# Performance work log

Hardware: AMD Instinct MI355X
Metric: run time of the kernel (lower is better)

## Reference

```python
import jax, jax.numpy as jnp
import numpy as np

POOLED_H = 7
POOLED_W = 7
SPATIAL_SCALE = 0.0625
IMG = 896  # image size -> 56x56 feature map at stride 16


def setup_inputs() -> dict:
    key = jax.random.key(0)
    kf, kb, kx1, kx2, ky1, ky2 = jax.random.split(key, 6)
    B, C, H, W = 4, 256, 56, 56
    N = 256
    features = jax.random.normal(kf, (B, C, H, W), dtype=jnp.float32)
    b = jax.random.randint(kb, (N,), 0, B)
    x1 = jax.random.randint(kx1, (N,), 0, IMG)
    y1 = jax.random.randint(ky1, (N,), 0, IMG)
    x2 = jnp.clip(x1 + jax.random.randint(kx2, (N,), 0, IMG), None, IMG - 1)
    y2 = jnp.clip(y1 + jax.random.randint(ky2, (N,), 0, IMG), None, IMG - 1)
    rois = jnp.stack([b, x1, y1, x2, y2], axis=1).astype(jnp.float32)
    return {"features": features, "rois": rois}


def reference(features, rois):
    # Faithful RoIPool (pool_type='MAX'):
    #   rois[:,1:] *= spatial_scale; rois = rois.long()  (truncation; coords >= 0 so == floor)
    #   crop features[b, :, y1:y2+1, x1:x2+1] and adaptive_max_pool2d to (7,7).
    B, C, H, W = features.shape
    N = rois.shape[0]
    r = rois.at[:, 1:].multiply(SPATIAL_SCALE).astype(jnp.int32)
    b, x1, y1, x2, y2 = r[:, 0], r[:, 1], r[:, 2], r[:, 3], r[:, 4]
    roi_h = y2 - y1 + 1  # crop uses y2+1 inclusive end
    roi_w = x2 - x1 + 1
    # adaptive pool bins for length L, out size o: start=floor(i*L/o), end=ceil((i+1)*L/o)
    # max bin width is bounded by ceil(H/o)+1, a static quantity -> jit friendly.
    MBH = -(-H // POOLED_H) + 1
    MBW = -(-W // POOLED_W) + 1
    ph = jnp.arange(POOLED_H)
    pw = jnp.arange(POOLED_W)

    hs = y1[:, None] + (ph[None, :] * roi_h[:, None]) // POOLED_H              # [N,7]
    he = y1[:, None] + ((ph[None, :] + 1) * roi_h[:, None] + POOLED_H - 1) // POOLED_H
    kh = jnp.arange(MBH)
    h_idx = jnp.clip(hs[:, :, None] + kh, 0, H - 1)                            # [N,7,MBH]
    h_valid = kh[None, None, :] < (he - hs)[:, :, None]                        # [N,7,MBH]

    ws = x1[:, None] + (pw[None, :] * roi_w[:, None]) // POOLED_W              # [N,7]
    we = x1[:, None] + ((pw[None, :] + 1) * roi_w[:, None] + POOLED_W - 1) // POOLED_W
    kw = jnp.arange(MBW)
    w_idx = jnp.clip(ws[:, :, None] + kw, 0, W - 1)                            # [N,7,MBW]
    w_valid = kw[None, None, :] < (we - ws)[:, :, None]                        # [N,7,MBW]

    fb = features[b]  # [N,C,H,W] per-ROI feature maps
    # max over the rectangle is separable: max over rows, then over cols.
    gh = jax.vmap(lambda f, hi: f[:, hi, :])(fb, h_idx)                        # [N,C,7,MBH,W]
    gh = jnp.where(h_valid[:, None, :, :, None], gh, -jnp.inf).max(axis=3)     # [N,C,7,W]
    gw = jax.vmap(lambda f, wi: f[:, :, wi])(gh, w_idx)                        # [N,C,7,7,MBW]
    out = jnp.where(w_valid[:, None, None, :, :], gw, -jnp.inf).max(axis=-1)   # [N,C,7,7]
    return out
```

## Files before the change

### kernel.cpp

```cpp
#include <hip/hip_runtime.h>
#include <math.h>

#define POOLED 7
#define SCALE 0.0625f
#define C_ 256
#define H_ 56
#define W_ 56
#define S_ (H_ * W_)
#define NCELL 49

typedef _Float16 f16x4 __attribute__((ext_vector_type(4)));

__device__ __forceinline__ f16x4 max4h(f16x4 a, f16x4 b) {
    f16x4 r;
    r[0] = a[0] > b[0] ? a[0] : b[0];
    r[1] = a[1] > b[1] ? a[1] : b[1];
    r[2] = a[2] > b[2] ? a[2] : b[2];
    r[3] = a[3] > b[3] ? a[3] : b[3];
    return r;
}

__global__ __launch_bounds__(1024) void nhwc_kernel(
    const float* __restrict__ src, _Float16* __restrict__ dst)
{
    __shared__ float tile[64][65];
    int b = blockIdx.z;
    int sbase = blockIdx.x * 64;
    int cbase = blockIdx.y * 64;
    int tid = threadIdx.x;

    const float* s0 = src + (size_t)b * C_ * S_;
    _Float16* d0 = dst + (size_t)b * S_ * C_;

    {
        int si = tid & 15;
        int c  = tid >> 4;
        float4 v = *(const float4*)(s0 + (size_t)(cbase + c) * S_ + sbase + 4 * si);
        tile[4 * si + 0][c] = v.x;
        tile[4 * si + 1][c] = v.y;
        tile[4 * si + 2][c] = v.z;
        tile[4 * si + 3][c] = v.w;
    }
    __syncthreads();
    {
        int cj = tid & 15;
        int s  = tid >> 4;
        f16x4 pk;
        pk[0] = (_Float16)tile[s][4 * cj + 0];
        pk[1] = (_Float16)tile[s][4 * cj + 1];
        pk[2] = (_Float16)tile[s][4 * cj + 2];
        pk[3] = (_Float16)tile[s][4 * cj + 3];
        *(f16x4*)(d0 + (size_t)(sbase + s) * C_ + cbase + 4 * cj) = pk;
    }
}

__global__ __launch_bounds__(256) void pool_kernel(
    const _Float16* __restrict__ t, const float* __restrict__ rois,
    float* __restrict__ ws2)
{
    int bid  = blockIdx.x;
    int swz  = (bid & 7) * 392 + (bid >> 3);
    int task = (threadIdx.x >> 6) * 3136 + swz;
    int lane = threadIdx.x & 63;

    int n    = task / NCELL;
    int cell = task % NCELL;
    int ph = cell / POOLED;
    int pw = cell % POOLED;

    const float* r = rois + n * 5;
    int b  = (int)r[0];
    int x1 = (int)(r[1] * SCALE);
    int y1 = (int)(r[2] * SCALE);
    int x2 = (int)(r[3] * SCALE);
    int y2 = (int)(r[4] * SCALE);
    int rh = y2 - y1 + 1;
    int rw = x2 - x1 + 1;

    int hs = y1 + (ph * rh) / POOLED;
    int he = y1 + ((ph + 1) * rh + POOLED - 1) / POOLED;
    int ws = x1 + (pw * rw) / POOLED;
    int we = x1 + ((pw + 1) * rw + POOLED - 1) / POOLED;
    int nh = he - hs;
    int nw = we - ws;

    const f16x4* p0 = (const f16x4*)(t + (size_t)b * S_ * C_) + lane
                      + (size_t)(hs * W_ + ws) * 64;

    const _Float16 NEGV = (_Float16)(-65504.0f);
    f16x4 a0 = {NEGV, NEGV, NEGV, NEGV};
    f16x4 a1 = a0, a2 = a0, a3 = a0, a4 = a0, a5 = a0, a6 = a0, a7 = a0;

    for (int h = 0; h < nh; h += 2) {
        int h1 = (h + 1 < nh) ? h + 1 : h;
        const f16x4* hp0 = p0 + (size_t)h  * (W_ * 64);
        const f16x4* hp1 = p0 + (size_t)h1 * (W_ * 64);
        for (int w = 0; w < nw; w += 4) {
            int w1 = (w + 1 < nw) ? w + 1 : w;
            int w2 = (w + 2 < nw) ? w + 2 : w;
            int w3 = (w + 3 < nw) ? w + 3 : w;
            a0 = max4h(a0, hp0[(size_t)w  * 64]);
            a1 = max4h(a1, hp0[(size_t)w1 * 64]);
            a2 = max4h(a2, hp0[(size_t)w2 * 64]);
            a3 = max4h(a3, hp0[(size_t)w3 * 64]);
            a4 = max4h(a4, hp1[(size_t)w  * 64]);
            a5 = max4h(a5, hp1[(size_t)w1 * 64]);
            a6 = max4h(a6, hp1[(size_t)w2 * 64]);
            a7 = max4h(a7, hp1[(size_t)w3 * 64]);
        }
    }
    f16x4 m = max4h(max4h(max4h(a0, a1), max4h(a2, a3)),
                    max4h(max4h(a4, a5), max4h(a6, a7)));

    float4 acc = make_float4((float)m[0], (float)m[1], (float)m[2], (float)m[3]);
    *((float4*)(ws2 + (size_t)task * C_) + lane) = acc;
}

__global__ __launch_bounds__(256) void outt_kernel(
    const float* __restrict__ ws2, float* __restrict__ out)
{
    __shared__ float tile[64][51];
    int n = blockIdx.x;
    int cbase = blockIdx.y * 64;
    int tid = threadIdx.x;

    const float* src = ws2 + (size_t)n * NCELL * C_;
    int cl = tid & 63;
    int cell0 = tid >> 6;
    #pragma unroll
    for (int k = 0; k < 13; ++k) {
        int cell = cell0 + 4 * k;
        if (cell < NCELL) tile[cl][cell] = src[(size_t)cell * C_ + cbase + cl];
    }
    __syncthreads();
    float* dst = out + (size_t)n * C_ * NCELL + (size_t)cbase * NCELL;
    #pragma unroll
    for (int k = 0; k < 13; ++k) {
        int f = tid + 256 * k;
        if (f < 64 * NCELL) {
            int c = f / NCELL, cell = f % NCELL;
            dst[f] = tile[c][cell];
        }
    }
}

__global__ __launch_bounds__(256) void roipool_direct_kernel(
    const float* __restrict__ feat, const float* __restrict__ rois,
    float* __restrict__ out, int total)
{
    int idx = blockIdx.x * blockDim.x + threadIdx.x;
    if (idx >= total) return;
    int pw = idx % POOLED;
    int ph = (idx / POOLED) % POOLED;
    int c  = (idx / (POOLED * POOLED)) % C_;
    int n  = idx / (POOLED * POOLED * C_);
    const float* r = rois + n * 5;
    int b  = (int)r[0];
    int x1 = (int)(r[1] * SCALE);
    int y1 = (int)(r[2] * SCALE);
    int x2 = (int)(r[3] * SCALE);
    int y2 = (int)(r[4] * SCALE);
    int rh = y2 - y1 + 1;
    int rw = x2 - x1 + 1;
    int hs = y1 + (ph * rh) / POOLED;
    int he = y1 + ((ph + 1) * rh + POOLED - 1) / POOLED;
    int ws = x1 + (pw * rw) / POOLED;
    int we = x1 + ((pw + 1) * rw + POOLED - 1) / POOLED;
    const float* plane = feat + ((size_t)b * C_ + c) * (size_t)S_;
    float m = -INFINITY;
    for (int h = hs; h < he; ++h) {
        const float* row = plane + h * W_;
        for (int w = ws; w < we; ++w) m = fmaxf(m, row[w]);
    }
    out[idx] = m;
}

extern "C" void kernel_launch(void* const* d_in, const int* in_sizes, int n_in,
                              void* d_out, int out_size, void* d_ws, size_t ws_size,
                              hipStream_t stream) {
    const float* feat = (const float*)d_in[0];
    const float* rois = (const float*)d_in[1];
    float* out = (float*)d_out;

    int N = in_sizes[1] / 5;
    size_t featBytes = (size_t)4 * S_ * C_ * sizeof(_Float16);
    size_t need = featBytes + (size_t)N * NCELL * C_ * sizeof(float);

    if (ws_size >= need && N == 256) {
        _Float16* t = (_Float16*)d_ws;
        float* ws2  = (float*)((char*)d_ws + featBytes);

        dim3 tgrid(S_ / 64, C_ / 64, 4);
        nhwc_kernel<<<tgrid, 1024, 0, stream>>>(feat, t);

        pool_kernel<<<3136, 256, 0, stream>>>(t, rois, ws2);

        dim3 ogrid(N, C_ / 64);
        outt_kernel<<<ogrid, 256, 0, stream>>>(ws2, out);
    } else {
        int total = N * C_ * POOLED * POOLED;
        roipool_direct_kernel<<<(total + 255) / 256, 256, 0, stream>>>(feat, rois, out, total);
    }
}
```

Measured before the change: 34.82 us.

## Fuse pooling and output transpose into one kernel via shared-memory staging

Each block now handles one ROI and a group of four pooled cells, one wave per cell. Results are staged in shared memory and written straight to the NCHW-ordered output. This removes the intermediate workspace buffer, its global write and read, and one kernel launch. In exchange the output stores are strided by 49 floats, so they are poorly coalesced. The last cell group has three idle waves, and the grid grows to 3328 blocks.

```diff
diff --git a/kernel.cpp b/kernel.cpp
--- a/kernel.cpp
+++ b/kernel.cpp
@@ -54,19 +54,18 @@
     }
 }
 
-__global__ __launch_bounds__(256) void pool_kernel(
+__global__ __launch_bounds__(256) void pool_fused_kernel(
     const _Float16* __restrict__ t, const float* __restrict__ rois,
-    float* __restrict__ ws2)
+    float* __restrict__ out)
 {
-    int bid  = blockIdx.x;
-    int swz  = (bid & 7) * 392 + (bid >> 3);
-    int task = (threadIdx.x >> 6) * 3136 + swz;
+    __shared__ float stage[4][257];
+    int b0   = blockIdx.x;
+    int swz  = (b0 & 7) * 416 + (b0 >> 3);
+    int n    = swz / 13;
+    int cg   = swz % 13;
+    int wv   = threadIdx.x >> 6;
     int lane = threadIdx.x & 63;
-
-    int n    = task / NCELL;
-    int cell = task % NCELL;
-    int ph = cell / POOLED;
-    int pw = cell % POOLED;
+    int cell = cg * 4 + wv;
 
     const float* r = rois + n * 5;
     int b  = (int)r[0];
@@ -77,70 +76,63 @@
     int rh = y2 - y1 + 1;
     int rw = x2 - x1 + 1;
 
-    int hs = y1 + (ph * rh) / POOLED;
-    int he = y1 + ((ph + 1) * rh + POOLED - 1) / POOLED;
-    int ws = x1 + (pw * rw) / POOLED;
-    int we = x1 + ((pw + 1) * rw + POOLED - 1) / POOLED;
-    int nh = he - hs;
-    int nw = we - ws;
+    if (cell < NCELL) {
+        int ph = cell / POOLED;
+        int pw = cell % POOLED;
+        int hs = y1 + (ph * rh) / POOLED;
+        int he = y1 + ((ph + 1) * rh + POOLED - 1) / POOLED;
+        int ws = x1 + (pw * rw) / POOLED;
+        int we = x1 + ((pw + 1) * rw + POOLED - 1) / POOLED;
+        int nh = he - hs;
+        int nw = we - ws;
 
-    const f16x4* p0 = (const f16x4*)(t + (size_t)b * S_ * C_) + lane
-                      + (size_t)(hs * W_ + ws) * 64;
+        const f16x4* p0 = (const f16x4*)(t + (size_t)b * S_ * C_) + lane
+                          + (size_t)(hs * W_ + ws) * 64;
 
-    const _Float16 NEGV = (_Float16)(-65504.0f);
-    f16x4 a0 = {NEGV, NEGV, NEGV, NEGV};
-    f16x4 a1 = a0, a2 = a0, a3 = a0, a4 = a0, a5 = a0, a6 = a0, a7 = a0;
+        const _Float16 NEGV = (_Float16)(-65504.0f);
+        f16x4 a0 = {NEGV, NEGV, NEGV, NEGV};
+        f16x4 a1 = a0, a2 = a0, a3 = a0, a4 = a0, a5 = a0, a6 = a0, a7 = a0;
 
-    for (int h = 0; h < nh; h += 2) {
-        int h1 = (h + 1 < nh) ? h + 1 : h;
-        const f16x4* hp0 = p0 + (size_t)h  * (W_ * 64);
-        const f16x4* hp1 = p0 + (size_t)h1 * (W_ * 64);
-        for (int w = 0; w < nw; w += 4) {
-            int w1 = (w + 1 < nw) ? w + 1 : w;
-            int w2 = (w + 2 < nw) ? w + 2 : w;
-            int w3 = (w + 3 < nw) ? w + 3 : w;
-            a0 = max4h(a0, hp0[(size_t)w  * 64]);
-            a1 = max4h(a1, hp0[(size_t)w1 * 64]);
-            a2 = max4h(a2, hp0[(size_t)w2 * 64]);
-            a3 = max4h(a3, hp0[(size_t)w3 * 64]);
-            a4 = max4h(a4, hp1[(size_t)w  * 64]);
-            a5 = max4h(a5, hp1[(size_t)w1 * 64]);
-            a6 = max4h(a6, hp1[(size_t)w2 * 64]);
-            a7 = max4h(a7, hp1[(size_t)w3 * 64]);
+        for (int h = 0; h < nh; h += 2) {
+            int h1 = (h + 1 < nh) ? h + 1 : h;
+            const f16x4* hp0 = p0 + (size_t)h  * (W_ * 64);
+            const f16x4* hp1 = p0 + (size_t)h1 * (W_ * 64);
+            for (int w = 0; w < nw; w += 4) {
+                int w1 = (w + 1 < nw) ? w + 1 : w;
+                int w2 = (w + 2 < nw) ? w + 2 : w;
+                int w3 = (w + 3 < nw) ? w + 3 : w;
+                a0 = max4h(a0, hp0[(size_t)w  * 64]);
+                a1 = max4h(a1, hp0[(size_t)w1 * 64]);
+                a2 = max4h(a2, hp0[(size_t)w2 * 64]);
+                a3 = max4h(a3, hp0[(size_t)w3 * 64]);
+                a4 = max4h(a4, hp1[(size_t)w  * 64]);
+                a5 = max4h(a5, hp1[(size_t)w1 * 64]);
+                a6 = max4h(a6, hp1[(size_t)w2 * 64]);
+                a7 = max4h(a7, hp1[(size_t)w3 * 64]);
+            }
         }
-    }
-    f16x4 m = max4h(max4h(max4h(a0, a1), max4h(a2, a3)),
-                    max4h(max4h(a4, a5), max4h(a6, a7)));
+        f16x4 m = max4h(max4h(max4h(a0, a1), max4h(a2, a3)),
+                        max4h(max4h(a4, a5), max4h(a6, a7)));
 
-    float4 acc = make_float4((float)m[0], (float)m[1], (float)m[2], (float)m[3]);
-    *((float4*)(ws2 + (size_t)task * C_) + lane) = acc;
-}
-
-__global__ __launch_bounds__(256) void outt_kernel(
-    const float* __restrict__ ws2, float* __restrict__ out)
-{
-    __shared__ float tile[64][51];
-    int n = blockIdx.x;
-    int cbase = blockIdx.y * 64;
-    int tid = threadIdx.x;
-
-    const float* src = ws2 + (size_t)n * NCELL * C_;
-    int cl = tid & 63;
-    int cell0 = tid >> 6;
-    #pragma unroll
-    for (int k = 0; k < 13; ++k) {
-        int cell = cell0 + 4 * k;
-        if (cell < NCELL) tile[cl][cell] = src[(size_t)cell * C_ + cbase + cl];
+        stage[wv][4 * lane + 0] = (float)m[0];
+        stage[wv][4 * lane + 1] = (float)m[1];
+        stage[wv][4 * lane + 2] = (float)m[2];
+        stage[wv][4 * lane + 3] = (float)m[3];
     }
     __syncthreads();
-    float* dst = out + (size_t)n * C_ * NCELL + (size_t)cbase * NCELL;
-    #pragma unroll
-    for (int k = 0; k < 13; ++k) {
-        int f = tid + 256 * k;
-        if (f < 64 * NCELL) {
-            int c = f / NCELL, cell = f % NCELL;
-            dst[f] = tile[c][cell];
+
+    float* dst = out + (size_t)n * C_ * NCELL + cg * 4;
+    int nc = (cg < 12) ? 4 : 1;
+    if (nc == 4) {
+        #pragma unroll
+        for (int k = 0; k < 4; ++k) {
+            int f = threadIdx.x + 256 * k;
+            int c = f >> 2, j = f & 3;
+            dst[(size_t)c * NCELL + j] = stage[j][c];
         }
+    } else {
+        int c = threadIdx.x;
+        dst[(size_t)c * NCELL] = stage[0][c];
     }
 }
 
@@ -184,19 +176,14 @@
 
     int N = in_sizes[1] / 5;
     size_t featBytes = (size_t)4 * S_ * C_ * sizeof(_Float16);
-    size_t need = featBytes + (size_t)N * NCELL * C_ * sizeof(float);
 
-    if (ws_size >= need && N == 256) {
+    if (ws_size >= featBytes && N == 256) {
         _Float16* t = (_Float16*)d_ws;
-        float* ws2  = (float*)((char*)d_ws + featBytes);
 
         dim3 tgrid(S_ / 64, C_ / 64, 4);
         nhwc_kernel<<<tgrid, 1024, 0, stream>>>(feat, t);
 
-        pool_kernel<<<3136, 256, 0, stream>>>(t, rois, ws2);
-
-        dim3 ogrid(N, C_ / 64);
-        outt_kernel<<<ogrid, 256, 0, stream>>>(ws2, out);
+        pool_fused_kernel<<<3328, 256, 0, stream>>>(t, rois, out);
     } else {
         int total = N * C_ * POOLED * POOLED;
         roipool_direct_kernel<<<(total + 255) / 256, 256, 0, stream>>>(feat, rois, out, total);
```

Measured after the change: 31.37 us. -9.9%, faster.
